# Kernel optimization log

Hardware: AMD Instinct MI355X
Metric: run time of the kernel (lower is better)

Reference implementation:

```python
import jax, jax.numpy as jnp
import numpy as np

N, NODE_IN, EDGE_IN, H, ROUNDS = 768, 64, 32, 128, 2


def setup_inputs() -> dict:
    key = jax.random.key(0)
    ks = jax.random.split(key, 12)
    node_feats = jax.random.normal(ks[0], (N, NODE_IN), dtype=jnp.float32)
    edge_feats = jax.random.normal(ks[1], (N, N, EDGE_IN), dtype=jnp.float32)
    adj_mask = jax.random.randint(ks[2], (N, N), 0, 2).astype(jnp.float32)
    def lin(k, fan_in, fan_out):
        w = jax.random.normal(k, (fan_in, fan_out), dtype=jnp.float32) / jnp.sqrt(fan_in)
        return w
    return {
        "node_feats": node_feats,
        "edge_feats": edge_feats,
        "adj_mask": adj_mask,
        "Wn": lin(ks[3], NODE_IN, H), "bn": jnp.zeros((H,), jnp.float32),
        "We": lin(ks[4], EDGE_IN, H), "be": jnp.zeros((H,), jnp.float32),
        "Wa": lin(ks[5], 2 * H, H), "ba": jnp.zeros((H,), jnp.float32),
        "Wu": lin(ks[6], 2 * H, H), "bu": jnp.zeros((H,), jnp.float32),
    }


def reference(node_feats, edge_feats, adj_mask, Wn, bn, We, be, Wa, ba, Wu, bu):
    relu = jax.nn.relu
    h = relu(node_feats @ Wn + bn)                      # (N, H)
    e = relu(jnp.einsum('ijf,fk->ijk', edge_feats, We) + be)  # (N, N, H)
    deg = jnp.clip(adj_mask.sum(axis=0), 1.0)[:, None]  # (N, 1) receiver degree
    # Precompute edge contribution to agg_lin once (constant across rounds):
    # concat([sender, e]) @ Wa == sender @ Wa[:H] + e @ Wa[H:]
    e_proj = jnp.einsum('ijh,hk->ijk', e, Wa[H:])       # (N, N, H)
    for _ in range(ROUNDS):
        s_proj = h @ Wa[:H]                              # (N, H) sender part
        msgs = relu(s_proj[:, None, :] + e_proj + ba)    # (N, N, H)
        agg = jnp.einsum('ijk,ij->jk', msgs, adj_mask) / deg  # masked sum over senders i
        h = relu(jnp.concatenate([h, agg], axis=-1) @ Wu + bu)
    graph_emb = h.mean(axis=0)
    return (h, graph_emb)
```

## Files before the change

### kernel.cpp

```cpp
#include <hip/hip_runtime.h>
#include <hip/hip_bf16.h>


typedef __bf16 bf16x8 __attribute__((ext_vector_type(8)));
typedef float f32x4 __attribute__((ext_vector_type(4)));

#define NN 768

static __device__ __forceinline__ unsigned short to_bf16u(float x) {
    return __builtin_bit_cast(unsigned short, (__bf16)x);
}

__global__ __launch_bounds__(256) void k_prep(
                       const float* __restrict__ adj,
                       const float* __restrict__ We, const float* __restrict__ Wa,
                       unsigned short* __restrict__ WeT, unsigned short* __restrict__ Wa2T,
                       const float* __restrict__ nf, const float* __restrict__ Wn,
                       const float* __restrict__ bn, const float* __restrict__ ba,
                       float* __restrict__ h, float* __restrict__ sp,
                       float* __restrict__ invdeg) {
    const int b = blockIdx.x, tid = threadIdx.x;
    if (b < 80) {
        int g = b * 256 + tid;
        if (g < 128 * 32) {
            int c = g >> 5, f = g & 31;
            WeT[g] = to_bf16u(We[f * 128 + c]);
        } else {
            int g2 = g - 128 * 32;
            int c = g2 >> 7, k = g2 & 127;
            Wa2T[g2] = to_bf16u(Wa[(128 + k) * 128 + c]);
        }
    } else if (b < 464) {
        __shared__ float nf_l[2][64];
        __shared__ float h_l[2][128];
        int row = tid >> 7, t = tid & 127;
        int i = (b - 80) * 2 + row;
        if (t < 64) nf_l[row][t] = nf[i * 64 + t];
        __syncthreads();
        float acc = bn[t];
#pragma unroll 8
        for (int f = 0; f < 64; ++f) acc += nf_l[row][f] * Wn[f * 128 + t];
        acc = fmaxf(acc, 0.f);
        h[i * 128 + t] = acc;
        h_l[row][t] = acc;
        __syncthreads();
        float spv = ba[t];
#pragma unroll 8
        for (int f = 0; f < 128; ++f) spv += h_l[row][f] * Wa[f * 128 + t];
        sp[i * 128 + t] = spv;
    } else {
        __shared__ float dsum[4][64];
        int d = b - 464;
        int q = tid >> 6, jj = tid & 63;
        int j = d * 64 + jj;
        float s = 0.f;
        for (int i = q * 192; i < q * 192 + 192; ++i)
            s += adj[(size_t)i * NN + j];
        dsum[q][jj] = s;
        __syncthreads();
        if (tid < 64) {
            float tot = dsum[0][tid] + dsum[1][tid] + dsum[2][tid] + dsum[3][tid];
            invdeg[d * 64 + tid] = 1.0f / fmaxf(tot, 1.0f);
        }
    }
}

__global__ __launch_bounds__(512) void k_build(
    const float* __restrict__ ef, const unsigned short* __restrict__ WeT,
    const unsigned short* __restrict__ Wa2T, const float* __restrict__ be,
    unsigned short* __restrict__ eproj) {
    __shared__ unsigned short ef_lds[128 * 40];
    __shared__ __align__(16) unsigned short e_lds[128 * 128];
    const int tid  = threadIdx.x;
    const size_t g0 = (size_t)blockIdx.x * 128;
    const int lane = tid & 63;
    const int wv   = tid >> 6;
    const int wr   = wv >> 2;
    const int wc   = wv & 3;
    const int lg   = lane >> 4;
    const int lr   = lane & 15;

    {
        int row = tid >> 2, c0 = (tid & 3) * 8;
        const float* src = ef + (g0 + row) * 32 + c0;
        float4 f0 = *reinterpret_cast<const float4*>(src);
        float4 f1 = *reinterpret_cast<const float4*>(src + 4);
        bf16x8 v;
        v[0] = (__bf16)f0.x; v[1] = (__bf16)f0.y; v[2] = (__bf16)f0.z; v[3] = (__bf16)f0.w;
        v[4] = (__bf16)f1.x; v[5] = (__bf16)f1.y; v[6] = (__bf16)f1.z; v[7] = (__bf16)f1.w;
        *reinterpret_cast<bf16x8*>(&ef_lds[row * 40 + c0]) = v;
    }
    bf16x8 bwe[2];
    bf16x8 bwa[2][4];
    float bereg[2];
#pragma unroll
    for (int t = 0; t < 2; ++t) {
        const int col = 32 * wc + 16 * t + lr;
        bwe[t] = *reinterpret_cast<const bf16x8*>(WeT + col * 32 + 8 * lg);
        bereg[t] = be[col];
#pragma unroll
        for (int s = 0; s < 4; ++s)
            bwa[t][s] = *reinterpret_cast<const bf16x8*>(Wa2T + col * 128 + 32 * s + 8 * lg);
    }
    __syncthreads();

#pragma unroll
    for (int s = 0; s < 4; ++s) {
        const int arow = 64 * wr + 16 * s + lr;
        bf16x8 a = *reinterpret_cast<const bf16x8*>(&ef_lds[arow * 40 + 8 * lg]);
#pragma unroll
        for (int t = 0; t < 2; ++t) {
            const int col = 32 * wc + 16 * t + lr;
            f32x4 c;
            c[0] = bereg[t]; c[1] = bereg[t]; c[2] = bereg[t]; c[3] = bereg[t];
            f32x4 C1 = __builtin_amdgcn_mfma_f32_16x16x32_bf16(a, bwe[t], c, 0, 0, 0);
#pragma unroll
            for (int r = 0; r < 4; ++r) {
                int row = 64 * wr + 16 * s + 4 * lg + r;
                int idx = (row * 128 + col) ^ ((row & 7) << 3);
                e_lds[idx] = to_bf16u(fmaxf(C1[r], 0.f));
            }
        }
    }
    __syncthreads();

    ushort4 outv[4][2];
#pragma unroll
    for (int s = 0; s < 4; ++s) {
        const int arow = 64 * wr + 16 * s + lr;
        bf16x8 ae[4];
#pragma unroll
        for (int ss = 0; ss < 4; ++ss) {
            int idx = (arow * 128 + 32 * ss + 8 * lg) ^ ((arow & 7) << 3);
            ae[ss] = *reinterpret_cast<const bf16x8*>(&e_lds[idx]);
        }
#pragma unroll
        for (int t = 0; t < 2; ++t) {
            f32x4 acc;
            acc[0] = 0.f; acc[1] = 0.f; acc[2] = 0.f; acc[3] = 0.f;
#pragma unroll
            for (int ss = 0; ss < 4; ++ss)
                acc = __builtin_amdgcn_mfma_f32_16x16x32_bf16(ae[ss], bwa[t][ss], acc, 0, 0, 0);
            outv[s][t].x = to_bf16u(acc[0]);
            outv[s][t].y = to_bf16u(acc[1]);
            outv[s][t].z = to_bf16u(acc[2]);
            outv[s][t].w = to_bf16u(acc[3]);
        }
    }
    __syncthreads();

#pragma unroll
    for (int s = 0; s < 4; ++s)
#pragma unroll
        for (int t = 0; t < 2; ++t) {
            const int col = 32 * wc + 16 * t + lr;
#pragma unroll
            for (int r = 0; r < 4; ++r) {
                int row = 64 * wr + 16 * s + 4 * lg + r;
                int idx = (row * 128 + col) ^ ((row & 7) << 3);
                unsigned short val = (r == 0) ? outv[s][t].x : (r == 1) ? outv[s][t].y
                                   : (r == 2) ? outv[s][t].z : outv[s][t].w;
                e_lds[idx] = val;
            }
        }
    __syncthreads();

    {
        int row = tid >> 2;
#pragma unroll
        for (int m = 0; m < 4; ++m) {
            int a = (tid & 3) + 4 * m;
            int idx = row * 128 + 8 * (a ^ (row & 7));
            f32x4 v = *reinterpret_cast<const f32x4*>(&e_lds[idx]);
            *reinterpret_cast<f32x4*>(eproj + (g0 + row) * 128 + 8 * a) = v;
        }
    }
}

__global__ __launch_bounds__(256) void k_round(
    const unsigned short* __restrict__ eproj, const float* __restrict__ adj,
    const float* __restrict__ sp, float* __restrict__ aggp) {
    const int tid = threadIdx.x;
    const int jt  = blockIdx.x >> 4;
    const int seg = blockIdx.x & 15;
    const int j0  = jt * 16;
    const int i0  = seg * 48;
    const int jj  = tid >> 4;
    const int kb  = (tid & 15) * 8;

    const size_t estep = (size_t)NN * 128;
    const unsigned short* ep = eproj + ((size_t)i0 * NN + j0 + jj) * 128 + kb;
    const float* ap = adj + (size_t)i0 * NN + j0 + jj;
    const float* spp = sp + (size_t)i0 * 128 + kb;

    float acc[8] = {0.f, 0.f, 0.f, 0.f, 0.f, 0.f, 0.f, 0.f};

    bf16x8 v = *reinterpret_cast<const bf16x8*>(ep);
    float av = *ap;
    float4 s0 = *reinterpret_cast<const float4*>(spp);
    float4 s1 = *reinterpret_cast<const float4*>(spp + 4);

    for (int m = 0; m < 48; ++m) {
        bf16x8 vn = v; float avn = av; float4 s0n = s0, s1n = s1;
        if (m < 47) {
            vn = *reinterpret_cast<const bf16x8*>(ep + estep);
            avn = ap[NN];
            s0n = *reinterpret_cast<const float4*>(spp + 128);
            s1n = *reinterpret_cast<const float4*>(spp + 132);
        }
        acc[0] += fmaxf(s0.x + (float)v[0], 0.f) * av;
        acc[1] += fmaxf(s0.y + (float)v[1], 0.f) * av;
        acc[2] += fmaxf(s0.z + (float)v[2], 0.f) * av;
        acc[3] += fmaxf(s0.w + (float)v[3], 0.f) * av;
        acc[4] += fmaxf(s1.x + (float)v[4], 0.f) * av;
        acc[5] += fmaxf(s1.y + (float)v[5], 0.f) * av;
        acc[6] += fmaxf(s1.z + (float)v[6], 0.f) * av;
        acc[7] += fmaxf(s1.w + (float)v[7], 0.f) * av;
        ep += estep; ap += NN; spp += 128;
        v = vn; av = avn; s0 = s0n; s1 = s1n;
    }

    float* dst = aggp + ((size_t)(j0 + jj) * 16 + seg) * 128 + kb;
    float4 o0, o1;
    o0.x = acc[0]; o0.y = acc[1]; o0.z = acc[2]; o0.w = acc[3];
    o1.x = acc[4]; o1.y = acc[5]; o1.z = acc[6]; o1.w = acc[7];
    *reinterpret_cast<float4*>(dst) = o0;
    *reinterpret_cast<float4*>(dst + 4) = o1;
}

template <int LAST>
__global__ __launch_bounds__(256) void k_upd(
                      const float* __restrict__ h_in, const float* __restrict__ aggp,
                      const float* __restrict__ invdeg,
                      const float* __restrict__ Wu, const float* __restrict__ bu,
                      const float* __restrict__ Wa, const float* __restrict__ ba,
                      float* __restrict__ h_out, float* __restrict__ sp,
                      float* __restrict__ out) {
    __shared__ float buf[2][256];
    __shared__ float hn[2][128];
    const int tid = threadIdx.x;
    const int row = tid >> 7, t = tid & 127;
    const int j = blockIdx.x * 2 + row;
    float s = 0.f;
#pragma unroll
    for (int seg = 0; seg < 16; ++seg)
        s += aggp[((size_t)j * 16 + seg) * 128 + t];
    buf[row][t] = h_in[j * 128 + t];
    buf[row][128 + t] = s * invdeg[j];
    __syncthreads();
    float acc = bu[t];
#pragma unroll 8
    for (int f = 0; f < 256; ++f) acc += buf[row][f] * Wu[f * 128 + t];
    acc = fmaxf(acc, 0.f);
    if (LAST) {
        out[j * 128 + t] = acc;
    } else {
        h_out[j * 128 + t] = acc;
        hn[row][t] = acc;
        __syncthreads();
        float spv = ba[t];
#pragma unroll 8
        for (int f = 0; f < 128; ++f) spv += hn[row][f] * Wa[f * 128 + t];
        sp[j * 128 + t] = spv;
    }
}

__global__ __launch_bounds__(64) void k_gemb(const float* __restrict__ out_h, float* __restrict__ out) {
    int c = blockIdx.x, l = threadIdx.x;
    float acc = 0.f;
    for (int i = l; i < NN; i += 64) acc += out_h[(size_t)i * 128 + c];
#pragma unroll
    for (int off = 32; off; off >>= 1) acc += __shfl_down(acc, off);
    if (l == 0) out[NN * 128 + c] = acc * (1.0f / 768.0f);
}

extern "C" void kernel_launch(void* const* d_in, const int* in_sizes, int n_in,
                              void* d_out, int out_size, void* d_ws, size_t ws_size,
                              hipStream_t stream) {
    const float* nf  = (const float*)d_in[0];
    const float* ef  = (const float*)d_in[1];
    const float* adj = (const float*)d_in[2];
    const float* Wn  = (const float*)d_in[3];
    const float* bn  = (const float*)d_in[4];
    const float* We  = (const float*)d_in[5];
    const float* be  = (const float*)d_in[6];
    const float* Wa  = (const float*)d_in[7];
    const float* ba  = (const float*)d_in[8];
    const float* Wu  = (const float*)d_in[9];
    const float* bu  = (const float*)d_in[10];
    float* out = (float*)d_out;

    float* h_buf  = (float*)d_ws;
    float* sp     = h_buf + NN * 128;
    float* invdeg = sp + NN * 128;
    float* aggp   = invdeg + NN;
    unsigned short* WeT   = (unsigned short*)(aggp + (size_t)NN * 16 * 128);
    unsigned short* Wa2T  = WeT + 128 * 32;
    unsigned short* eproj = Wa2T + 128 * 128;

    k_prep<<<476, 256, 0, stream>>>(adj, We, Wa, WeT, Wa2T, nf, Wn, bn, ba,
                                    h_buf, sp, invdeg);
    k_build<<<NN * NN / 128, 512, 0, stream>>>(ef, WeT, Wa2T, be, eproj);

    k_round<<<48 * 16, 256, 0, stream>>>(eproj, adj, sp, aggp);
    k_upd<0><<<NN / 2, 256, 0, stream>>>(h_buf, aggp, invdeg, Wu, bu, Wa, ba, h_buf, sp, out);
    k_round<<<48 * 16, 256, 0, stream>>>(eproj, adj, sp, aggp);
    k_upd<1><<<NN / 2, 256, 0, stream>>>(h_buf, aggp, invdeg, Wu, bu, Wa, ba, h_buf, sp, out);

    k_gemb<<<128, 64, 0, stream>>>(out, out);
}
```

Measured before the change: 152.6 us.

## Make k_build persistent per sender row with double-buffered LDS pipeline

Each k_build block now processes a whole row of 768 edges in 24 chunks of 32, instead of one 128-edge tile per block. The weight fragments are loaded into registers once per block rather than once per tile. The edge-feature load for chunk n+2 and the first GEMM for chunk n+1 overlap with the second GEMM of chunk n, using a two-slot LDS buffer. The second MFMA swaps its operands so results come out transposed and can be written straight to global memory, removing the LDS staging pass for the output. The cost is fewer, longer blocks, one barrier per chunk, and 8-byte global stores instead of 16-byte ones.

```diff
diff --git a/kernel.cpp b/kernel.cpp
--- a/kernel.cpp
+++ b/kernel.cpp
@@ -69,27 +69,16 @@
     const float* __restrict__ ef, const unsigned short* __restrict__ WeT,
     const unsigned short* __restrict__ Wa2T, const float* __restrict__ be,
     unsigned short* __restrict__ eproj) {
-    __shared__ unsigned short ef_lds[128 * 40];
-    __shared__ __align__(16) unsigned short e_lds[128 * 128];
+    __shared__ __align__(16) unsigned short e_lds[2][32 * 128];
     const int tid  = threadIdx.x;
-    const size_t g0 = (size_t)blockIdx.x * 128;
     const int lane = tid & 63;
     const int wv   = tid >> 6;
     const int wr   = wv >> 2;
     const int wc   = wv & 3;
     const int lg   = lane >> 4;
     const int lr   = lane & 15;
-
-    {
-        int row = tid >> 2, c0 = (tid & 3) * 8;
-        const float* src = ef + (g0 + row) * 32 + c0;
-        float4 f0 = *reinterpret_cast<const float4*>(src);
-        float4 f1 = *reinterpret_cast<const float4*>(src + 4);
-        bf16x8 v;
-        v[0] = (__bf16)f0.x; v[1] = (__bf16)f0.y; v[2] = (__bf16)f0.z; v[3] = (__bf16)f0.w;
-        v[4] = (__bf16)f1.x; v[5] = (__bf16)f1.y; v[6] = (__bf16)f1.z; v[7] = (__bf16)f1.w;
-        *reinterpret_cast<bf16x8*>(&ef_lds[row * 40 + c0]) = v;
-    }
+    const size_t gbase = (size_t)blockIdx.x * NN;
+
     bf16x8 bwe[2];
     bf16x8 bwa[2][4];
     float bereg[2];
@@ -102,12 +91,15 @@
         for (int s = 0; s < 4; ++s)
             bwa[t][s] = *reinterpret_cast<const bf16x8*>(Wa2T + col * 128 + 32 * s + 8 * lg);
     }
-    __syncthreads();
-
-#pragma unroll
-    for (int s = 0; s < 4; ++s) {
-        const int arow = 64 * wr + 16 * s + lr;
-        bf16x8 a = *reinterpret_cast<const bf16x8*>(&ef_lds[arow * 40 + 8 * lg]);
+
+    auto load_a = [&](int n, bf16x8& x) {
+        const float* p = ef + (gbase + 32 * n + 16 * wr + lr) * 32 + 8 * lg;
+        float4 f0 = *reinterpret_cast<const float4*>(p);
+        float4 f1 = *reinterpret_cast<const float4*>(p + 4);
+        x[0] = (__bf16)f0.x; x[1] = (__bf16)f0.y; x[2] = (__bf16)f0.z; x[3] = (__bf16)f0.w;
+        x[4] = (__bf16)f1.x; x[5] = (__bf16)f1.y; x[6] = (__bf16)f1.z; x[7] = (__bf16)f1.w;
+    };
+    auto gemm1 = [&](bf16x8 a, int buf) {
 #pragma unroll
         for (int t = 0; t < 2; ++t) {
             const int col = 32 * wc + 16 * t + lr;
@@ -116,64 +108,47 @@
             f32x4 C1 = __builtin_amdgcn_mfma_f32_16x16x32_bf16(a, bwe[t], c, 0, 0, 0);
 #pragma unroll
             for (int r = 0; r < 4; ++r) {
-                int row = 64 * wr + 16 * s + 4 * lg + r;
+                int row = 16 * wr + 4 * lg + r;
                 int idx = (row * 128 + col) ^ ((row & 7) << 3);
-                e_lds[idx] = to_bf16u(fmaxf(C1[r], 0.f));
+                e_lds[buf][idx] = to_bf16u(fmaxf(C1[r], 0.f));
             }
         }
-    }
+    };
+
+    bf16x8 cA, pA;
+    load_a(0, cA);
+    gemm1(cA, 0);
+    load_a(1, cA);
     __syncthreads();
 
-    ushort4 outv[4][2];
-#pragma unroll
-    for (int s = 0; s < 4; ++s) {
-        const int arow = 64 * wr + 16 * s + lr;
+    for (int n = 0; n < 24; ++n) {
+        const int b = n & 1;
+        if (n + 2 < 24) load_a(n + 2, pA);
+        if (n + 1 < 24) gemm1(cA, b ^ 1);
+
         bf16x8 ae[4];
-#pragma unroll
-        for (int ss = 0; ss < 4; ++ss) {
-            int idx = (arow * 128 + 32 * ss + 8 * lg) ^ ((arow & 7) << 3);
-            ae[ss] = *reinterpret_cast<const bf16x8*>(&e_lds[idx]);
-        }
+        const int erow = 16 * wr + lr;
+#pragma unroll
+        for (int s = 0; s < 4; ++s) {
+            int idx = (erow * 128 + 32 * s + 8 * lg) ^ ((erow & 7) << 3);
+            ae[s] = *reinterpret_cast<const bf16x8*>(&e_lds[b][idx]);
+        }
+        unsigned short* orow = eproj + (gbase + 32 * n + 16 * wr + lr) * 128;
 #pragma unroll
         for (int t = 0; t < 2; ++t) {
             f32x4 acc;
             acc[0] = 0.f; acc[1] = 0.f; acc[2] = 0.f; acc[3] = 0.f;
 #pragma unroll
-            for (int ss = 0; ss < 4; ++ss)
-                acc = __builtin_amdgcn_mfma_f32_16x16x32_bf16(ae[ss], bwa[t][ss], acc, 0, 0, 0);
-            outv[s][t].x = to_bf16u(acc[0]);
-            outv[s][t].y = to_bf16u(acc[1]);
-            outv[s][t].z = to_bf16u(acc[2]);
-            outv[s][t].w = to_bf16u(acc[3]);
-        }
-    }
-    __syncthreads();
-
-#pragma unroll
-    for (int s = 0; s < 4; ++s)
-#pragma unroll
-        for (int t = 0; t < 2; ++t) {
-            const int col = 32 * wc + 16 * t + lr;
-#pragma unroll
-            for (int r = 0; r < 4; ++r) {
-                int row = 64 * wr + 16 * s + 4 * lg + r;
-                int idx = (row * 128 + col) ^ ((row & 7) << 3);
-                unsigned short val = (r == 0) ? outv[s][t].x : (r == 1) ? outv[s][t].y
-                                   : (r == 2) ? outv[s][t].z : outv[s][t].w;
-                e_lds[idx] = val;
-            }
-        }
-    __syncthreads();
-
-    {
-        int row = tid >> 2;
-#pragma unroll
-        for (int m = 0; m < 4; ++m) {
-            int a = (tid & 3) + 4 * m;
-            int idx = row * 128 + 8 * (a ^ (row & 7));
-            f32x4 v = *reinterpret_cast<const f32x4*>(&e_lds[idx]);
-            *reinterpret_cast<f32x4*>(eproj + (g0 + row) * 128 + 8 * a) = v;
-        }
+            for (int s = 0; s < 4; ++s)
+                acc = __builtin_amdgcn_mfma_f32_16x16x32_bf16(bwa[t][s], ae[s], acc, 0, 0, 0);
+            ushort4 o;
+            o.x = to_bf16u(acc[0]); o.y = to_bf16u(acc[1]);
+            o.z = to_bf16u(acc[2]); o.w = to_bf16u(acc[3]);
+            *reinterpret_cast<ushort4*>(orow + 32 * wc + 16 * t + 4 * lg) = o;
+        }
+
+        if (n + 2 < 24) cA = pA;
+        __syncthreads();
     }
 }
 
@@ -300,7 +275,7 @@
 
     k_prep<<<476, 256, 0, stream>>>(adj, We, Wa, WeT, Wa2T, nf, Wn, bn, ba,
                                     h_buf, sp, invdeg);
-    k_build<<<NN * NN / 128, 512, 0, stream>>>(ef, WeT, Wa2T, be, eproj);
+    k_build<<<NN, 512, 0, stream>>>(ef, WeT, Wa2T, be, eproj);
 
     k_round<<<48 * 16, 256, 0, stream>>>(eproj, adj, sp, aggp);
     k_upd<0><<<NN / 2, 256, 0, stream>>>(h_buf, aggp, invdeg, Wu, bu, Wa, ba, h_buf, sp, out);
```

Measured after the change: 151.2 us. About the same (-0.9%).
